# Kernel tuning notes

Measured on AMD Instinct MI355X. Metric: run time of the kernel, lower is better.

The kernel has to match this reference:

```python
import jax, jax.numpy as jnp
import numpy as np

T_VALUES = (2.0, 8.0, 32.0, 128.0)
EPS = 1e-05
N_BANDS = 128


def setup_inputs() -> dict:
    key = jax.random.key(0)
    k1, k2, k3, k4 = jax.random.split(key, 4)
    x = jax.random.uniform(k1, (8, N_BANDS, 8192), dtype=jnp.float32)
    # Parameters are stored in log-space, matching the torch module's init
    # (log(alpha), log(delta), log(r) broadcast to n_bands).
    log_alpha = jnp.full((N_BANDS,), np.log(0.8), dtype=jnp.float32)
    log_delta = jnp.full((N_BANDS,), np.log(10.0), dtype=jnp.float32)
    log_r = jnp.full((N_BANDS,), np.log(0.25), dtype=jnp.float32)
    return {"x": x, "log_alpha": log_alpha, "log_delta": log_delta, "log_r": log_r}


def reference(x, log_alpha, log_delta, log_r):
    # x: [B, F, N]  (batch, bands, time frames)
    t_vals = jnp.asarray(T_VALUES, dtype=x.dtype)
    # s = (sqrt(1 + 4 t^2) - 1) / (2 t^2)  -- smoothing coefficient per rate
    s_vals = (jnp.sqrt(1.0 + 4.0 * t_vals ** 2) - 1.0) / (2.0 * t_vals ** 2)

    alpha = jnp.exp(log_alpha)[:, None]  # [F, 1]
    delta = jnp.exp(log_delta)[:, None]
    r = jnp.exp(log_r)[:, None]

    xt = jnp.moveaxis(x, -1, 0)  # [N, B, F], scan over time

    def ema(s):
        # IIR recursion m[t] = s*x[t] + (1-s)*m[t-1], m[-1] = x[0].
        # This is exactly what the torch triangular-matmul formulation computes:
        # smoother[t] = s * sum_{i<=t} x[i] (1-s)^{t-i} + (1-s)^{t+1} x[0].
        def step(m, xi):
            m = s * xi + (1.0 - s) * m
            return m, m
        _, ys = jax.lax.scan(step, xt[0], xt)
        return jnp.moveaxis(ys, 0, -1)  # [B, F, N]

    smoother = jax.vmap(ema)(s_vals)  # [T, B, F, N]

    # smooth = (eps + smoother)^(-alpha), written as in the source via log1p
    smooth = jnp.exp(-alpha * (jnp.log(EPS) + jnp.log1p(smoother / EPS)))
    pcen = (x[None] * smooth + delta) ** r - delta ** r  # [T, B, F, N]
    return jnp.transpose(pcen, (1, 0, 2, 3))  # [B, T, F, N]
```

## Files before the change

kernel.cpp:

```cpp
#include <hip/hip_runtime.h>

#define NB    128
#define NT    8192
#define TPB   512
#define CHUNK 16

__device__ __forceinline__ float fexp2(float x) { return __builtin_amdgcn_exp2f(x); }
__device__ __forceinline__ float flog2(float x) { return __builtin_amdgcn_logf(x); }

__device__ __forceinline__ int swz(int n) { return n ^ (((n >> 5) & 7) << 2); }

__global__ __launch_bounds__(TPB, 8) void mrpcen_kernel(
    const float* __restrict__ x,
    const float* __restrict__ log_alpha,
    const float* __restrict__ log_delta,
    const float* __restrict__ log_r,
    float* __restrict__ out)
{
    __shared__ __align__(16) float sh[NT];
    __shared__ float sWagg[8];

    const int tid  = threadIdx.x;
    const int lane = tid & 63;
    const int wid  = tid >> 6;

    const int bft = blockIdx.x;
    const int t   = bft & 3;
    const int f   = (bft >> 2) & (NB - 1);
    const int b   = bft >> 9;

    const float* xrow = x + (size_t)(b * NB + f) * NT;

    const float alpha  = __expf(log_alpha[f]);
    const float r      = __expf(log_r[f]);
    const float delta  = __expf(log_delta[f]);
    const float deltar = __expf(r * log_delta[f]);
    const float nalpha = -alpha;

    const float tt = (float)(2 << (2 * t));
    const float t2 = tt * tt;
    const float s  = (sqrtf(1.f + 4.f * t2) - 1.f) / (2.f * t2);
    const float a1 = 1.f - s;
    float A = a1;
    A = A * A; A = A * A; A = A * A; A = A * A;

    float xc[CHUNK];
#pragma unroll
    for (int j = 0; j < 4; j++) {
        float4 v = *reinterpret_cast<const float4*>(xrow + tid * CHUNK + 4 * j);
        xc[4 * j + 0] = v.x; xc[4 * j + 1] = v.y;
        xc[4 * j + 2] = v.z; xc[4 * j + 3] = v.w;
    }
    const float x0 = xrow[0];

    float Bl = 0.f;
#pragma unroll
    for (int i = 0; i < CHUNK; i++)
        Bl = s * xc[i] + a1 * Bl;

    float v = Bl;
    float ap = A;
#pragma unroll
    for (int d = 1; d < 64; d <<= 1) {
        float up = __shfl_up(v, d);
        if (lane >= d) v += ap * up;
        ap *= ap;
    }
    const float a64 = ap;
    if (lane == 63) sWagg[wid] = v;
    __syncthreads();

    float pre = 0.f;
#pragma unroll
    for (int k = 0; k < 7; k++)
        if (wid > k) pre = a64 * pre + sWagg[k];

    float pl = 1.f, base = A;
    int e = lane;
#pragma unroll
    for (int bit = 0; bit < 6; bit++) {
        if (e & 1) pl *= base;
        base *= base;
        e >>= 1;
    }
    float aw = 1.f, wb = a64;
    e = wid;
#pragma unroll
    for (int bit = 0; bit < 3; bit++) {
        if (e & 1) aw *= wb;
        wb *= wb;
        e >>= 1;
    }

    const float vprev = __shfl_up(v, 1);
    float m = pl * (aw * x0 + pre) + ((lane > 0) ? vprev : 0.f);

#pragma unroll
    for (int j = 0; j < 4; j++) {
        float ov[4];
#pragma unroll
        for (int q = 0; q < 4; q++) {
            float xi = xc[4 * j + q];
            m = s * xi + a1 * m;
            float smooth = fexp2(nalpha * flog2(1e-5f + m));
            ov[q] = fexp2(r * flog2(xi * smooth + delta)) - deltar;
        }
        *reinterpret_cast<float4*>(&sh[swz(tid * CHUNK + 4 * j)]) =
            make_float4(ov[0], ov[1], ov[2], ov[3]);
    }

    float* oplane = out + (((size_t)b * 4 + t) * NB + f) * (size_t)NT;
    const int wbase = wid << 10;
#pragma unroll
    for (int k = 0; k < 4; k++) {
        int n = wbase + k * 256 + lane * 4;
        float4 o = *reinterpret_cast<const float4*>(&sh[swz(n)]);
        *reinterpret_cast<float4*>(oplane + n) = o;
    }
}

extern "C" void kernel_launch(void* const* d_in, const int* in_sizes, int n_in,
                              void* d_out, int out_size, void* d_ws, size_t ws_size,
                              hipStream_t stream) {
    const float* x         = (const float*)d_in[0];
    const float* log_alpha = (const float*)d_in[1];
    const float* log_delta = (const float*)d_in[2];
    const float* log_r     = (const float*)d_in[3];
    float* out = (float*)d_out;

    mrpcen_kernel<<<dim3(8 * NB * 4), dim3(TPB), 0, stream>>>(
        x, log_alpha, log_delta, log_r, out);
}
```

Before: 163.8 us.

## Compute all four smoothing rates per block to reuse loaded input row

Measured after the change: 234.5 us. +43.2%, slower.

```diff
diff --git a/kernel.cpp b/kernel.cpp
--- a/kernel.cpp
+++ b/kernel.cpp
@@ -4,6 +4,7 @@
 #define NT    8192
 #define TPB   512
 #define CHUNK 16
+#define NRATE 4
 
 __device__ __forceinline__ float fexp2(float x) { return __builtin_amdgcn_exp2f(x); }
 __device__ __forceinline__ float flog2(float x) { return __builtin_amdgcn_logf(x); }
@@ -18,18 +19,17 @@
     float* __restrict__ out)
 {
     __shared__ __align__(16) float sh[NT];
-    __shared__ float sWagg[8];
+    __shared__ float4 sWagg[8];
 
     const int tid  = threadIdx.x;
     const int lane = tid & 63;
     const int wid  = tid >> 6;
 
-    const int bft = blockIdx.x;
-    const int t   = bft & 3;
-    const int f   = (bft >> 2) & (NB - 1);
-    const int b   = bft >> 9;
+    const int bf = blockIdx.x;
+    const int b  = bf >> 7;
+    const int f  = bf & (NB - 1);
 
-    const float* xrow = x + (size_t)(b * NB + f) * NT;
+    const float* xrow = x + (size_t)bf * NT;
 
     const float alpha  = __expf(log_alpha[f]);
     const float r      = __expf(log_r[f]);
@@ -37,85 +37,107 @@
     const float deltar = __expf(r * log_delta[f]);
     const float nalpha = -alpha;
 
-    const float tt = (float)(2 << (2 * t));
-    const float t2 = tt * tt;
-    const float s  = (sqrtf(1.f + 4.f * t2) - 1.f) / (2.f * t2);
-    const float a1 = 1.f - s;
-    float A = a1;
-    A = A * A; A = A * A; A = A * A; A = A * A;
+    float s[NRATE], A[NRATE];
+#pragma unroll
+    for (int t = 0; t < NRATE; t++) {
+        const float tt = (float)(2 << (2 * t));
+        const float t2 = tt * tt;
+        s[t] = (sqrtf(1.f + 4.f * t2) - 1.f) / (2.f * t2);
+        float a = 1.f - s[t];
+        a = a * a; a = a * a; a = a * a; a = a * a;
+        A[t] = a;
+    }
 
     float xc[CHUNK];
 #pragma unroll
     for (int j = 0; j < 4; j++) {
-        float4 v = *reinterpret_cast<const float4*>(xrow + tid * CHUNK + 4 * j);
-        xc[4 * j + 0] = v.x; xc[4 * j + 1] = v.y;
-        xc[4 * j + 2] = v.z; xc[4 * j + 3] = v.w;
+        float4 v4 = *reinterpret_cast<const float4*>(xrow + tid * CHUNK + 4 * j);
+        xc[4 * j + 0] = v4.x; xc[4 * j + 1] = v4.y;
+        xc[4 * j + 2] = v4.z; xc[4 * j + 3] = v4.w;
     }
     const float x0 = xrow[0];
 
-    float Bl = 0.f;
+    float v[NRATE] = {0.f, 0.f, 0.f, 0.f};
 #pragma unroll
-    for (int i = 0; i < CHUNK; i++)
-        Bl = s * xc[i] + a1 * Bl;
+    for (int i = 0; i < CHUNK; i++) {
+        const float xi = xc[i];
+#pragma unroll
+        for (int t = 0; t < NRATE; t++)
+            v[t] = s[t] * xi + (1.f - s[t]) * v[t];
+    }
 
-    float v = Bl;
-    float ap = A;
+    float ap[NRATE] = {A[0], A[1], A[2], A[3]};
 #pragma unroll
     for (int d = 1; d < 64; d <<= 1) {
-        float up = __shfl_up(v, d);
-        if (lane >= d) v += ap * up;
-        ap *= ap;
+#pragma unroll
+        for (int t = 0; t < NRATE; t++) {
+            const float up = __shfl_up(v[t], d);
+            if (lane >= d) v[t] += ap[t] * up;
+            ap[t] *= ap[t];
+        }
     }
-    const float a64 = ap;
-    if (lane == 63) sWagg[wid] = v;
+    if (lane == 63) sWagg[wid] = make_float4(v[0], v[1], v[2], v[3]);
     __syncthreads();
 
-    float pre = 0.f;
+    float m_in[NRATE];
+    {
+        float pre[NRATE] = {0.f, 0.f, 0.f, 0.f};
 #pragma unroll
-    for (int k = 0; k < 7; k++)
-        if (wid > k) pre = a64 * pre + sWagg[k];
-
-    float pl = 1.f, base = A;
-    int e = lane;
+        for (int k = 0; k < 7; k++) {
+            if (wid > k) {
+                const float4 w4 = sWagg[k];
+                pre[0] = ap[0] * pre[0] + w4.x;
+                pre[1] = ap[1] * pre[1] + w4.y;
+                pre[2] = ap[2] * pre[2] + w4.z;
+                pre[3] = ap[3] * pre[3] + w4.w;
+            }
+        }
 #pragma unroll
-    for (int bit = 0; bit < 6; bit++) {
-        if (e & 1) pl *= base;
-        base *= base;
-        e >>= 1;
-    }
-    float aw = 1.f, wb = a64;
-    e = wid;
+        for (int t = 0; t < NRATE; t++) {
+            float pl = 1.f, base = A[t];
+            int e = lane;
 #pragma unroll
-    for (int bit = 0; bit < 3; bit++) {
-        if (e & 1) aw *= wb;
-        wb *= wb;
-        e >>= 1;
+            for (int bit = 0; bit < 6; bit++) {
+                if (e & 1) pl *= base;
+                base *= base; e >>= 1;
+            }
+            float aw = 1.f, wb = ap[t];
+            int ew = wid;
+#pragma unroll
+            for (int bit = 0; bit < 3; bit++) {
+                if (ew & 1) aw *= wb;
+                wb *= wb; ew >>= 1;
+            }
+            const float vprev = __shfl_up(v[t], 1);
+            m_in[t] = pl * (aw * x0 + pre[t]) + ((lane > 0) ? vprev : 0.f);
+        }
     }
 
-    const float vprev = __shfl_up(v, 1);
-    float m = pl * (aw * x0 + pre) + ((lane > 0) ? vprev : 0.f);
-
-#pragma unroll
-    for (int j = 0; j < 4; j++) {
-        float ov[4];
-#pragma unroll
-        for (int q = 0; q < 4; q++) {
-            float xi = xc[4 * j + q];
-            m = s * xi + a1 * m;
-            float smooth = fexp2(nalpha * flog2(1e-5f + m));
-            ov[q] = fexp2(r * flog2(xi * smooth + delta)) - deltar;
-        }
-        *reinterpret_cast<float4*>(&sh[swz(tid * CHUNK + 4 * j)]) =
-            make_float4(ov[0], ov[1], ov[2], ov[3]);
-    }
-
-    float* oplane = out + (((size_t)b * 4 + t) * NB + f) * (size_t)NT;
     const int wbase = wid << 10;
 #pragma unroll
-    for (int k = 0; k < 4; k++) {
-        int n = wbase + k * 256 + lane * 4;
-        float4 o = *reinterpret_cast<const float4*>(&sh[swz(n)]);
-        *reinterpret_cast<float4*>(oplane + n) = o;
+    for (int t = 0; t < NRATE; t++) {
+        const float st = s[t], a1 = 1.f - s[t];
+        float m = m_in[t];
+#pragma unroll
+        for (int j = 0; j < 4; j++) {
+            float ov[4];
+#pragma unroll
+            for (int q = 0; q < 4; q++) {
+                const float xi = xc[4 * j + q];
+                m = st * xi + a1 * m;
+                const float smooth = fexp2(nalpha * flog2(1e-5f + m));
+                ov[q] = fexp2(r * flog2(xi * smooth + delta)) - deltar;
+            }
+            *reinterpret_cast<float4*>(&sh[swz(tid * CHUNK + 4 * j)]) =
+                make_float4(ov[0], ov[1], ov[2], ov[3]);
+        }
+        float* oplane = out + (((size_t)b * 4 + t) * NB + f) * (size_t)NT;
+#pragma unroll
+        for (int k = 0; k < 4; k++) {
+            const int n = wbase + k * 256 + lane * 4;
+            float4 o = *reinterpret_cast<const float4*>(&sh[swz(n)]);
+            *reinterpret_cast<float4*>(oplane + n) = o;
+        }
     }
 }
 
@@ -128,6 +150,6 @@
     const float* log_r     = (const float*)d_in[3];
     float* out = (float*)d_out;
 
-    mrpcen_kernel<<<dim3(8 * NB * 4), dim3(TPB), 0, stream>>>(
+    mrpcen_kernel<<<dim3(8 * NB), dim3(TPB), 0, stream>>>(
         x, log_alpha, log_delta, log_r, out);
 }
```
